# Performance work log

Hardware: AMD Instinct MI355X
Metric: run time of the kernel (lower is better)

## Reference

```python
import jax, jax.numpy as jnp
import numpy as np

N = 64          # Hilbert space dim
B = 4096        # batch of density matrices
K = 2           # number of jump operators
DT = 0.01       # time step
C = (0.0, 0.5, 1.0)
A = ((0.0, 0.0, 0.0), (0.5, 0.0, 0.0), (0.0, 1.0, 0.0))
BW = (1.0 / 6.0, 2.0 / 3.0, 1.0 / 6.0)
NEUMANN_ORDER = 2


def _dag(M):
    # real-valued reference: dagger == transpose on last two axes
    return jnp.swapaxes(M, -1, -2)


def _sandwich(M, rho):
    # M rho M^dag ; M:[N,N], rho:[B,N,N]
    return M @ rho @ _dag(M)


def _dissipator(L, rho):
    # sum_k L_k rho L_k^dag ; L:[K,N,N], rho:[B,N,N]
    return jnp.einsum('kij,bjl,kml->bim', L, rho, L)


def _neumann_ratio(Ui, Uj, I):
    # U(ci) U(cj)^{-1} with U(cj)^{-1} ~ sum_{p<=order} (I - U(cj))^p
    W = I - Uj
    inv = I
    Wp = I
    for _ in range(NEUMANN_ORDER):
        Wp = Wp @ W
        inv = inv + Wp
    return Ui @ inv


def _forward(rho0, U_half, U_one, L0, Lh, L1):
    I = jnp.eye(N, dtype=rho0.dtype)
    Umap = {0.0: I, 0.5: U_half, 1.0: U_one}
    Lmap = {0.0: L0, 0.5: Lh, 1.0: L1}

    def ratio(ci, cj):
        if ci == cj:
            return I
        if cj == 0.0:
            return Umap[ci]
        return _neumann_ratio(Umap[ci], Umap[cj], I)

    # intermediate stages rho^(i)
    stages = []
    for i, ci in enumerate(C):
        rho_i = rho0 if ci == 0.0 else _sandwich(Umap[ci], rho0)
        for j in range(i):
            a_ij = A[i][j]
            if a_ij == 0.0:
                continue
            cj = C[j]
            P_ij = ratio(ci, cj)
            rho_i = rho_i + DT * a_ij * _sandwich(P_ij, _dissipator(Lmap[cj], stages[j]))
        stages.append(rho_i)

    # output combination
    rho_new = _sandwich(Umap[1.0], rho0)
    for i, bi in enumerate(BW):
        if bi == 0.0:
            continue
        ci = C[i]
        Q_i = ratio(1.0, ci)
        rho_new = rho_new + DT * bi * _sandwich(Q_i, _dissipator(Lmap[ci], stages[i]))
    return rho_new


def setup_inputs() -> dict:
    key = jax.random.key(0)
    k1, k2, k3, k4, k5, k6 = jax.random.split(key, 6)
    I = jnp.eye(N, dtype=jnp.float32)
    rho0 = jax.random.normal(k1, (B, N, N), dtype=jnp.float32)
    rho0 = 0.5 * (rho0 + jnp.swapaxes(rho0, -1, -2))  # hermitian-like
    # no-jump propagators: near-identity so the Neumann series is sane
    U_half = I + 0.02 * jax.random.normal(k2, (N, N), dtype=jnp.float32)
    U_one = I + 0.04 * jax.random.normal(k3, (N, N), dtype=jnp.float32)
    L0 = 0.1 * jax.random.normal(k4, (K, N, N), dtype=jnp.float32)
    Lh = 0.1 * jax.random.normal(k5, (K, N, N), dtype=jnp.float32)
    L1 = 0.1 * jax.random.normal(k6, (K, N, N), dtype=jnp.float32)
    return {"rho0": rho0, "U_half": U_half, "U_one": U_one,
            "L0": L0, "Lh": Lh, "L1": L1}


def reference(rho0, U_half, U_one, L0, Lh, L1):
    return _forward(rho0, U_half, U_one, L0, Lh, L1)
```

## Files before the change

### kernel.cpp

```cpp
#include <hip/hip_runtime.h>
#include <hip/hip_bf16.h>

#define NDIM 64
#define BP   72
#define DT_  0.01f
#define NTERM 7

typedef __attribute__((ext_vector_type(8)))  short bf16x8;
typedef __attribute__((ext_vector_type(16))) float f32x16;

struct Frag { bf16x8 f[4]; };


__device__ __forceinline__ unsigned short f2b(float x) {
    __hip_bfloat16 h = __float2bfloat16(x);
    return __builtin_bit_cast(unsigned short, h);
}
__device__ __forceinline__ float b2f(unsigned short u) {
    unsigned int v = (unsigned int)u << 16;
    return __builtin_bit_cast(float, v);
}
__device__ __forceinline__ unsigned int f2b2(float lo, float hi) {
    return (unsigned int)f2b(lo) | ((unsigned int)f2b(hi) << 16);
}

__device__ __forceinline__ void plswap(unsigned int& a, unsigned int& b) {
    asm("v_permlane32_swap_b32 %0, %1" : "+v"(a), "+v"(b));
}


__device__ __forceinline__ bf16x8 ldfrag(const unsigned short* M, int rb, int j, int ln, int hq) {
    return *(const bf16x8*)&M[(rb + ln) * BP + j * 16 + hq * 8];
}

__device__ __forceinline__ void ldg_op(Frag& F, const unsigned short* __restrict__ p,
                                       int ln, int hq, int cw) {
#pragma unroll
    for (int j = 0; j < 4; ++j)
        F.f[j] = *(const bf16x8*)&p[(cw + ln) * 64 + j * 16 + hq * 8];
}

__device__ __forceinline__ void ldsF(Frag& F, const unsigned short* p, int ln, int hq, int cw) {
#pragma unroll
    for (int j = 0; j < 4; ++j)
        F.f[j] = *(const bf16x8*)&p[(cw + ln) * BP + j * 16 + hq * 8];
}

__device__ __forceinline__ void ldg_opF32(Frag& F, const float* __restrict__ P,
                                          int ln, int hq, int cw) {
    const int n = cw + ln;
#pragma unroll
    for (int j = 0; j < 4; ++j) {
        const float* q = &P[n * 64 + j * 16 + hq * 8];
        float4 u = *(const float4*)q;
        float4 v = *(const float4*)(q + 4);
        uint4 o;
        o.x = f2b2(u.x, u.y); o.y = f2b2(u.z, u.w);
        o.z = f2b2(v.x, v.y); o.w = f2b2(v.z, v.w);
        F.f[j] = __builtin_bit_cast(bf16x8, o);
    }
}

__device__ __forceinline__ void ldWfrag(Frag& F, const float* __restrict__ Uh,
                                        int ln, int hq, int cw) {
    const int n = cw + ln;
#pragma unroll
    for (int j = 0; j < 4; ++j) {
        const int k0 = j * 16 + hq * 8;
        const float* q = &Uh[n * 64 + k0];
        float4 u = *(const float4*)q;
        float4 v = *(const float4*)(q + 4);
        float wv[8] = {-u.x, -u.y, -u.z, -u.w, -v.x, -v.y, -v.z, -v.w};
#pragma unroll
        for (int e = 0; e < 8; ++e)
            if (n == k0 + e) wv[e] += 1.f;
        uint4 o;
        o.x = f2b2(wv[0], wv[1]); o.y = f2b2(wv[2], wv[3]);
        o.z = f2b2(wv[4], wv[5]); o.w = f2b2(wv[6], wv[7]);
        F.f[j] = __builtin_bit_cast(bf16x8, o);
    }
}

template <bool ACC>
__device__ __forceinline__ void ntg(const unsigned short* A, const Frag& F, f32x16& acc,
                                    int ln, int hq, int rb) {
    if (!ACC) {
#pragma unroll
        for (int r = 0; r < 16; ++r) acc[r] = 0.f;
    }
#pragma unroll
    for (int j = 0; j < 4; ++j)
        acc = __builtin_amdgcn_mfma_f32_32x32x16_bf16(ldfrag(A, rb, j, ln, hq), F.f[j], acc, 0, 0, 0);
}

__device__ __forceinline__ f32x16 ntg_reg(const Frag& A, const Frag& F, const f32x16& Z) {
    f32x16 a = __builtin_amdgcn_mfma_f32_32x32x16_bf16(A.f[0], F.f[0], Z, 0, 0, 0);
#pragma unroll
    for (int j = 1; j < 4; ++j)
        a = __builtin_amdgcn_mfma_f32_32x32x16_bf16(A.f[j], F.f[j], a, 0, 0, 0);
    return a;
}

__device__ __forceinline__ void stN(unsigned short* D, const f32x16& v,
                                    int ln, int hq, int rw, int cw) {
#pragma unroll
    for (int r = 0; r < 16; ++r) {
        int row = rw + (r & 3) + 8 * (r >> 2) + 4 * hq;
        D[row * BP + (cw + ln)] = f2b(v[r]);
    }
}

__device__ __forceinline__ void ldT(float* r, const unsigned short* S,
                                    int ln, int hq, int rw, int cw) {
#pragma unroll
    for (int g = 0; g < 4; ++g) {
        uint2 u = *(const uint2*)&S[(cw + ln) * BP + rw + 8 * g + 4 * hq];
        unsigned short o[4];
        *(uint2*)o = u;
#pragma unroll
        for (int j = 0; j < 4; ++j) r[4 * g + j] = b2f(o[j]);
    }
}

__device__ __forceinline__ void emit(unsigned short* __restrict__ g, const f32x16& v, float s,
                                     int ln, int hq, int rw, int cw) {
#pragma unroll
    for (int gq = 0; gq < 4; ++gq) {
        uint2 o;
        o.x = f2b2(s * v[4 * gq + 0], s * v[4 * gq + 1]);
        o.y = f2b2(s * v[4 * gq + 2], s * v[4 * gq + 3]);
        *(uint2*)&g[(cw + ln) * 64 + rw + 8 * gq + 4 * hq] = o;
    }
}


__global__ void __launch_bounds__(256) krk_setup(const float* __restrict__ Uh,
                                                 const float* __restrict__ U1,
                                                 const float* __restrict__ L0,
                                                 const float* __restrict__ Lh,
                                                 const float* __restrict__ L1,
                                                 unsigned short* __restrict__ ws) {
    __shared__ unsigned short B[7][NDIM * BP];

    const int tid = threadIdx.x;
    const int lane = tid & 63, w = tid >> 6, ln = lane & 31, hq = lane >> 5;
    const int rw = 32 * (w >> 1), cw = 32 * (w & 1);

    const float c16 = DT_ / 6.f, c23 = 2.f * DT_ / 3.f;
    const float sA = sqrtf(c16);
    const float sB = sqrtf(c23);

#pragma unroll
    for (int i = 0; i < 4; ++i) {
        int flat = (tid + i * 256) * 4;
        int r = flat >> 6, c = flat & 63;
        float4 u = *(const float4*)&Uh[flat];
        const float* uf = (const float*)&u;
        float wv[4];
#pragma unroll
        for (int j = 0; j < 4; ++j) wv[j] = ((r == c + j) ? 1.f : 0.f) - uf[j];
#pragma unroll
        for (int j = 0; j < 4; ++j) B[0][(c + j) * BP + r] = f2b(uf[j]);
        uint2 ow; ow.x = f2b2(wv[0], wv[1]); ow.y = f2b2(wv[2], wv[3]);
        *(uint2*)&B[4][r * BP + c] = ow;
#pragma unroll
        for (int j = 0; j < 4; ++j) B[5][(c + j) * BP + r] = f2b(wv[j]);

        float4 p = *(const float4*)&U1[flat];
        const float* pf = (const float*)&p;
#pragma unroll
        for (int j = 0; j < 4; ++j) B[1][(c + j) * BP + r] = f2b(pf[j]);
        uint2 oq; oq.x = f2b2(p.x, p.y); oq.y = f2b2(p.z, p.w);
        *(uint2*)&ws[flat] = oq;

        float4 a = *(const float4*)&L0[flat];
        const float* af = (const float*)&a;
#pragma unroll
        for (int j = 0; j < 4; ++j) B[2][(c + j) * BP + r] = f2b(af[j]);
        float4 b = *(const float4*)&L0[4096 + flat];
        const float* bf = (const float*)&b;
#pragma unroll
        for (int j = 0; j < 4; ++j) B[3][(c + j) * BP + r] = f2b(bf[j]);
    }

    Frag FUh, FU1, FLh0, FLh1, F10, F11, Fw;
    ldg_opF32(FUh,  Uh,        ln, hq, cw);
    ldg_opF32(FU1,  U1,        ln, hq, cw);
    ldg_opF32(FLh0, Lh,        ln, hq, cw);
    ldg_opF32(FLh1, Lh + 4096, ln, hq, cw);
    ldg_opF32(F10,  L1,        ln, hq, cw);
    ldg_opF32(F11,  L1 + 4096, ln, hq, cw);
    ldWfrag(Fw, Uh, ln, hq, cw);
    __syncthreads();

    f32x16 e;

    {
        f32x16 t0;
        ntg<false>(B[5], Fw, t0, ln, hq, rw);
        float wts[16];
        ldT(wts, B[4], ln, hq, rw, cw);
#pragma unroll
        for (int g = 0; g < 4; ++g) {
            float vv[4];
#pragma unroll
            for (int i = 0; i < 4; ++i) {
                int r = 4 * g + i;
                int row = rw + i + 8 * g + 4 * hq;
                vv[i] = ((row == cw + ln) ? 1.f : 0.f) + wts[r] + t0[r];
            }
            uint2 o; o.x = f2b2(vv[0], vv[1]); o.y = f2b2(vv[2], vv[3]);
            *(uint2*)&B[6][(cw + ln) * BP + rw + 8 * g + 4 * hq] = o;
        }
    }
    ntg<false>(B[2], FU1, e, ln, hq, rw); emit(ws + 1 * 4096, e, sA, ln, hq, rw, cw);
    ntg<false>(B[3], FU1, e, ln, hq, rw); emit(ws + 2 * 4096, e, sA, ln, hq, rw, cw);
    ntg<false>(B[1], F10, e, ln, hq, rw); emit(ws + 5 * 4096, e, sA, ln, hq, rw, cw);
    ntg<false>(B[1], F11, e, ln, hq, rw); emit(ws + 6 * 4096, e, sA, ln, hq, rw, cw);
    __syncthreads();

    Frag FV; ldsF(FV, B[6], ln, hq, cw);

    ntg<false>(B[0], FLh0, e, ln, hq, rw); stN(B[2], e, ln, hq, rw, cw);
    ntg<false>(B[0], FLh1, e, ln, hq, rw); stN(B[3], e, ln, hq, rw, cw);
    __syncthreads();

    ntg<false>(B[2], FV, e, ln, hq, rw); stN(B[4], e, ln, hq, rw, cw);
    ntg<false>(B[3], FV, e, ln, hq, rw); stN(B[5], e, ln, hq, rw, cw);
    __syncthreads();

    ntg<false>(B[4], FU1, e, ln, hq, rw); emit(ws + 3 * 4096, e, sB, ln, hq, rw, cw);
    ntg<false>(B[5], FU1, e, ln, hq, rw); emit(ws + 4 * 4096, e, sB, ln, hq, rw, cw);
}


__global__ void __launch_bounds__(256, 2) krk_main(const float* __restrict__ rho0,
                                                   const unsigned short* __restrict__ ws,
                                                   float* __restrict__ out) {
    const int tid = threadIdx.x;
    const int w = tid >> 6, lane = tid & 63, ln = lane & 31, hq = lane >> 5;

    const int mat = 4 * blockIdx.x + w;
    const float* rho = rho0 + (size_t)mat * 4096;

    Frag Ar[2];
#pragma unroll
    for (int kb = 0; kb < 2; ++kb)
#pragma unroll
        for (int j = 0; j < 4; ++j) {
            const float* q = &rho[(kb * 32 + ln) * 64 + j * 16 + hq * 8];
            float4 u = *(const float4*)q;
            float4 v = *(const float4*)(q + 4);
            uint4 o;
            o.x = f2b2(u.x, u.y); o.y = f2b2(u.z, u.w);
            o.z = f2b2(v.x, v.y); o.w = f2b2(v.z, v.w);
            Ar[kb].f[j] = __builtin_bit_cast(bf16x8, o);
        }

    f32x16 Z;
#pragma unroll
    for (int r = 0; r < 16; ++r) Z[r] = 0.f;
    f32x16 acc00 = Z, acc01 = Z, acc10 = Z, acc11 = Z;

    Frag F[2][2];
    ldg_op(F[0][0], ws, ln, hq, 0);
    ldg_op(F[0][1], ws, ln, hq, 32);

#pragma unroll
    for (int t = 0; t < NTERM; ++t) {
        const int cur = t & 1, nxt = cur ^ 1;
        if (t + 1 < NTERM) {
            ldg_op(F[nxt][0], ws + (size_t)(t + 1) * 4096, ln, hq, 0);
            ldg_op(F[nxt][1], ws + (size_t)(t + 1) * 4096, ln, hq, 32);
        }
#pragma unroll
        for (int c = 0; c < 2; ++c) {
            Frag afr;
#pragma unroll
            for (int kb = 0; kb < 2; ++kb) {
                f32x16 T = ntg_reg(Ar[kb], F[cur][c], Z);
                unsigned int P[8];
#pragma unroll
                for (int p = 0; p < 8; ++p) P[p] = f2b2(T[2 * p], T[2 * p + 1]);
                plswap(P[0], P[2]); plswap(P[1], P[3]);
                plswap(P[4], P[6]); plswap(P[5], P[7]);
                uint4 lo; lo.x = P[0]; lo.y = P[1]; lo.z = P[2]; lo.w = P[3];
                uint4 hi; hi.x = P[4]; hi.y = P[5]; hi.z = P[6]; hi.w = P[7];
                afr.f[2 * kb]     = __builtin_bit_cast(bf16x8, lo);
                afr.f[2 * kb + 1] = __builtin_bit_cast(bf16x8, hi);
            }
#pragma unroll
            for (int j = 0; j < 4; ++j) {
                f32x16& a0 = c ? acc10 : acc00;
                f32x16& a1 = c ? acc11 : acc01;
                a0 = __builtin_amdgcn_mfma_f32_32x32x16_bf16(afr.f[j], F[cur][0].f[j], a0, 0, 0, 0);
                a1 = __builtin_amdgcn_mfma_f32_32x32x16_bf16(afr.f[j], F[cur][1].f[j], a1, 0, 0, 0);
            }
        }
    }

    float* o = out + (size_t)mat * 4096;
#pragma unroll
    for (int I = 0; I < 2; ++I)
#pragma unroll
        for (int J = 0; J < 2; ++J) {
            const f32x16& a = I ? (J ? acc11 : acc10) : (J ? acc01 : acc00);
#pragma unroll
            for (int g = 0; g < 4; ++g) {
                float4 v;
                v.x = a[4 * g + 0]; v.y = a[4 * g + 1];
                v.z = a[4 * g + 2]; v.w = a[4 * g + 3];
                *(float4*)&o[(J * 32 + ln) * 64 + I * 32 + 8 * g + 4 * hq] = v;
            }
        }
}


extern "C" void kernel_launch(void* const* d_in, const int* in_sizes, int n_in,
                              void* d_out, int out_size, void* d_ws, size_t ws_size,
                              hipStream_t stream) {
    const float* rho0 = (const float*)d_in[0];
    const float* Uh   = (const float*)d_in[1];
    const float* U1   = (const float*)d_in[2];
    const float* L0   = (const float*)d_in[3];
    const float* Lh   = (const float*)d_in[4];
    const float* L1   = (const float*)d_in[5];
    float* out = (float*)d_out;
    unsigned short* ws = (unsigned short*)d_ws;

    int Bn = in_sizes[0] / (NDIM * NDIM);

    krk_setup<<<1, 256, 0, stream>>>(Uh, U1, L0, Lh, L1, ws);
    krk_main<<<Bn / 4, 256, 0, stream>>>(rho0, ws, out);
}
```

Before: 161.6 us.

## Split setup across three blocks and split terms across two waves per matrix

The setup kernel is spread over three blocks: one emits the L0 and L1 based factors, the other two each compute one Lh based factor. The main kernel now uses one block of two waves per density matrix. Each wave handles a subset of the seven rank-one terms (4 and 3), and the partial accumulators are reduced through shared memory. This adds parallelism to the serial setup and gives more waves per matrix, at the cost of an LDS reduction and barriers, and with the term work split unevenly between the two waves.

```diff
diff --git a/kernel.cpp b/kernel.cpp
--- a/kernel.cpp
+++ b/kernel.cpp
@@ -142,7 +142,7 @@
                                                  unsigned short* __restrict__ ws) {
     __shared__ unsigned short B[7][NDIM * BP];
 
-    const int tid = threadIdx.x;
+    const int blk = blockIdx.x, tid = threadIdx.x;
     const int lane = tid & 63, w = tid >> 6, ln = lane & 31, hq = lane >> 5;
     const int rw = 32 * (w >> 1), cw = 32 * (w & 1);
 
@@ -171,7 +171,7 @@
 #pragma unroll
         for (int j = 0; j < 4; ++j) B[1][(c + j) * BP + r] = f2b(pf[j]);
         uint2 oq; oq.x = f2b2(p.x, p.y); oq.y = f2b2(p.z, p.w);
-        *(uint2*)&ws[flat] = oq;
+        if (blk == 0) *(uint2*)&ws[flat] = oq;
 
         float4 a = *(const float4*)&L0[flat];
         const float* af = (const float*)&a;
@@ -183,21 +183,30 @@
         for (int j = 0; j < 4; ++j) B[3][(c + j) * BP + r] = f2b(bf[j]);
     }
 
-    Frag FUh, FU1, FLh0, FLh1, F10, F11, Fw;
-    ldg_opF32(FUh,  Uh,        ln, hq, cw);
-    ldg_opF32(FU1,  U1,        ln, hq, cw);
-    ldg_opF32(FLh0, Lh,        ln, hq, cw);
-    ldg_opF32(FLh1, Lh + 4096, ln, hq, cw);
-    ldg_opF32(F10,  L1,        ln, hq, cw);
-    ldg_opF32(F11,  L1 + 4096, ln, hq, cw);
-    ldWfrag(Fw, Uh, ln, hq, cw);
+    Frag FU1, Fa, Fb;
+    ldg_opF32(FU1, U1, ln, hq, cw);
+    if (blk == 0) {
+        ldg_opF32(Fa, L1,        ln, hq, cw);
+        ldg_opF32(Fb, L1 + 4096, ln, hq, cw);
+    } else {
+        ldWfrag(Fa, Uh, ln, hq, cw);
+        ldg_opF32(Fb, (blk == 1) ? Lh : Lh + 4096, ln, hq, cw);
+    }
     __syncthreads();
 
     f32x16 e;
+
+    if (blk == 0) {
+        ntg<false>(B[2], FU1, e, ln, hq, rw); emit(ws + 1 * 4096, e, sA, ln, hq, rw, cw);
+        ntg<false>(B[3], FU1, e, ln, hq, rw); emit(ws + 2 * 4096, e, sA, ln, hq, rw, cw);
+        ntg<false>(B[1], Fa,  e, ln, hq, rw); emit(ws + 5 * 4096, e, sA, ln, hq, rw, cw);
+        ntg<false>(B[1], Fb,  e, ln, hq, rw); emit(ws + 6 * 4096, e, sA, ln, hq, rw, cw);
+        return;
+    }
 
     {
         f32x16 t0;
-        ntg<false>(B[5], Fw, t0, ln, hq, rw);
+        ntg<false>(B[5], Fa, t0, ln, hq, rw);
         float wts[16];
         ldT(wts, B[4], ln, hq, rw, cw);
 #pragma unroll
@@ -213,35 +222,29 @@
             *(uint2*)&B[6][(cw + ln) * BP + rw + 8 * g + 4 * hq] = o;
         }
     }
-    ntg<false>(B[2], FU1, e, ln, hq, rw); emit(ws + 1 * 4096, e, sA, ln, hq, rw, cw);
-    ntg<false>(B[3], FU1, e, ln, hq, rw); emit(ws + 2 * 4096, e, sA, ln, hq, rw, cw);
-    ntg<false>(B[1], F10, e, ln, hq, rw); emit(ws + 5 * 4096, e, sA, ln, hq, rw, cw);
-    ntg<false>(B[1], F11, e, ln, hq, rw); emit(ws + 6 * 4096, e, sA, ln, hq, rw, cw);
+    __syncthreads();
+
+    ntg<false>(B[0], Fb, e, ln, hq, rw); stN(B[2], e, ln, hq, rw, cw);
     __syncthreads();
 
     Frag FV; ldsF(FV, B[6], ln, hq, cw);
-
-    ntg<false>(B[0], FLh0, e, ln, hq, rw); stN(B[2], e, ln, hq, rw, cw);
-    ntg<false>(B[0], FLh1, e, ln, hq, rw); stN(B[3], e, ln, hq, rw, cw);
-    __syncthreads();
-
     ntg<false>(B[2], FV, e, ln, hq, rw); stN(B[4], e, ln, hq, rw, cw);
-    ntg<false>(B[3], FV, e, ln, hq, rw); stN(B[5], e, ln, hq, rw, cw);
-    __syncthreads();
-
-    ntg<false>(B[4], FU1, e, ln, hq, rw); emit(ws + 3 * 4096, e, sB, ln, hq, rw, cw);
-    ntg<false>(B[5], FU1, e, ln, hq, rw); emit(ws + 4 * 4096, e, sB, ln, hq, rw, cw);
-}
-
-
-__global__ void __launch_bounds__(256, 2) krk_main(const float* __restrict__ rho0,
+    __syncthreads();
+
+    ntg<false>(B[4], FU1, e, ln, hq, rw);
+    emit(ws + (size_t)(blk == 1 ? 3 : 4) * 4096, e, sB, ln, hq, rw, cw);
+}
+
+
+__global__ void __launch_bounds__(128, 2) krk_main(const float* __restrict__ rho0,
                                                    const unsigned short* __restrict__ ws,
                                                    float* __restrict__ out) {
+    __shared__ float xch[2][16][64];
+
     const int tid = threadIdx.x;
     const int w = tid >> 6, lane = tid & 63, ln = lane & 31, hq = lane >> 5;
 
-    const int mat = 4 * blockIdx.x + w;
-    const float* rho = rho0 + (size_t)mat * 4096;
+    const float* rho = rho0 + (size_t)blockIdx.x * 4096;
 
     Frag Ar[2];
 #pragma unroll
@@ -262,57 +265,82 @@
     for (int r = 0; r < 16; ++r) Z[r] = 0.f;
     f32x16 acc00 = Z, acc01 = Z, acc10 = Z, acc11 = Z;
 
+    const int tbase = w ? 4 : 0;
+    const int tcnt  = w ? 3 : 4;
+
     Frag F[2][2];
-    ldg_op(F[0][0], ws, ln, hq, 0);
-    ldg_op(F[0][1], ws, ln, hq, 32);
-
-#pragma unroll
-    for (int t = 0; t < NTERM; ++t) {
-        const int cur = t & 1, nxt = cur ^ 1;
-        if (t + 1 < NTERM) {
-            ldg_op(F[nxt][0], ws + (size_t)(t + 1) * 4096, ln, hq, 0);
-            ldg_op(F[nxt][1], ws + (size_t)(t + 1) * 4096, ln, hq, 32);
-        }
-#pragma unroll
-        for (int c = 0; c < 2; ++c) {
-            Frag afr;
-#pragma unroll
-            for (int kb = 0; kb < 2; ++kb) {
-                f32x16 T = ntg_reg(Ar[kb], F[cur][c], Z);
-                unsigned int P[8];
-#pragma unroll
-                for (int p = 0; p < 8; ++p) P[p] = f2b2(T[2 * p], T[2 * p + 1]);
-                plswap(P[0], P[2]); plswap(P[1], P[3]);
-                plswap(P[4], P[6]); plswap(P[5], P[7]);
-                uint4 lo; lo.x = P[0]; lo.y = P[1]; lo.z = P[2]; lo.w = P[3];
-                uint4 hi; hi.x = P[4]; hi.y = P[5]; hi.z = P[6]; hi.w = P[7];
-                afr.f[2 * kb]     = __builtin_bit_cast(bf16x8, lo);
-                afr.f[2 * kb + 1] = __builtin_bit_cast(bf16x8, hi);
+    ldg_op(F[0][0], ws + (size_t)tbase * 4096, ln, hq, 0);
+    ldg_op(F[0][1], ws + (size_t)tbase * 4096, ln, hq, 32);
+
+#pragma unroll
+    for (int i = 0; i < 4; ++i) {
+        if (i < tcnt) {
+            const int cur = i & 1, nxt = cur ^ 1;
+            if (i + 1 < tcnt) {
+                ldg_op(F[nxt][0], ws + (size_t)(tbase + i + 1) * 4096, ln, hq, 0);
+                ldg_op(F[nxt][1], ws + (size_t)(tbase + i + 1) * 4096, ln, hq, 32);
             }
 #pragma unroll
-            for (int j = 0; j < 4; ++j) {
-                f32x16& a0 = c ? acc10 : acc00;
-                f32x16& a1 = c ? acc11 : acc01;
-                a0 = __builtin_amdgcn_mfma_f32_32x32x16_bf16(afr.f[j], F[cur][0].f[j], a0, 0, 0, 0);
-                a1 = __builtin_amdgcn_mfma_f32_32x32x16_bf16(afr.f[j], F[cur][1].f[j], a1, 0, 0, 0);
+            for (int c = 0; c < 2; ++c) {
+                Frag afr;
+#pragma unroll
+                for (int kb = 0; kb < 2; ++kb) {
+                    f32x16 T = ntg_reg(Ar[kb], F[cur][c], Z);
+                    unsigned int P[8];
+#pragma unroll
+                    for (int p = 0; p < 8; ++p) P[p] = f2b2(T[2 * p], T[2 * p + 1]);
+                    plswap(P[0], P[2]); plswap(P[1], P[3]);
+                    plswap(P[4], P[6]); plswap(P[5], P[7]);
+                    uint4 lo; lo.x = P[0]; lo.y = P[1]; lo.z = P[2]; lo.w = P[3];
+                    uint4 hi; hi.x = P[4]; hi.y = P[5]; hi.z = P[6]; hi.w = P[7];
+                    afr.f[2 * kb]     = __builtin_bit_cast(bf16x8, lo);
+                    afr.f[2 * kb + 1] = __builtin_bit_cast(bf16x8, hi);
+                }
+#pragma unroll
+                for (int j = 0; j < 4; ++j) {
+                    f32x16& a0 = c ? acc10 : acc00;
+                    f32x16& a1 = c ? acc11 : acc01;
+                    a0 = __builtin_amdgcn_mfma_f32_32x32x16_bf16(afr.f[j], F[cur][0].f[j], a0, 0, 0, 0);
+                    a1 = __builtin_amdgcn_mfma_f32_32x32x16_bf16(afr.f[j], F[cur][1].f[j], a1, 0, 0, 0);
+                }
             }
         }
     }
 
-    float* o = out + (size_t)mat * 4096;
-#pragma unroll
-    for (int I = 0; I < 2; ++I)
-#pragma unroll
-        for (int J = 0; J < 2; ++J) {
-            const f32x16& a = I ? (J ? acc11 : acc10) : (J ? acc01 : acc00);
-#pragma unroll
-            for (int g = 0; g < 4; ++g) {
-                float4 v;
-                v.x = a[4 * g + 0]; v.y = a[4 * g + 1];
-                v.z = a[4 * g + 2]; v.w = a[4 * g + 3];
-                *(float4*)&o[(J * 32 + ln) * 64 + I * 32 + 8 * g + 4 * hq] = v;
+    if (w == 1) {
+#pragma unroll
+        for (int r = 0; r < 16; ++r) { xch[0][r][lane] = acc00[r]; xch[1][r][lane] = acc01[r]; }
+    }
+    __syncthreads();
+    if (w == 0) {
+#pragma unroll
+        for (int r = 0; r < 16; ++r) { acc00[r] += xch[0][r][lane]; acc01[r] += xch[1][r][lane]; }
+    }
+    __syncthreads();
+    if (w == 1) {
+#pragma unroll
+        for (int r = 0; r < 16; ++r) { xch[0][r][lane] = acc10[r]; xch[1][r][lane] = acc11[r]; }
+    }
+    __syncthreads();
+    if (w == 0) {
+#pragma unroll
+        for (int r = 0; r < 16; ++r) { acc10[r] += xch[0][r][lane]; acc11[r] += xch[1][r][lane]; }
+
+        float* o = out + (size_t)blockIdx.x * 4096;
+#pragma unroll
+        for (int I = 0; I < 2; ++I)
+#pragma unroll
+            for (int J = 0; J < 2; ++J) {
+                const f32x16& a = I ? (J ? acc11 : acc10) : (J ? acc01 : acc00);
+#pragma unroll
+                for (int g = 0; g < 4; ++g) {
+                    float4 v;
+                    v.x = a[4 * g + 0]; v.y = a[4 * g + 1];
+                    v.z = a[4 * g + 2]; v.w = a[4 * g + 3];
+                    *(float4*)&o[(J * 32 + ln) * 64 + I * 32 + 8 * g + 4 * hq] = v;
+                }
             }
-        }
+    }
 }
 
 
@@ -330,6 +358,6 @@
 
     int Bn = in_sizes[0] / (NDIM * NDIM);
 
-    krk_setup<<<1, 256, 0, stream>>>(Uh, U1, L0, Lh, L1, ws);
-    krk_main<<<Bn / 4, 256, 0, stream>>>(rho0, ws, out);
-}
+    krk_setup<<<3, 256, 0, stream>>>(Uh, U1, L0, Lh, L1, ws);
+    krk_main<<<Bn, 128, 0, stream>>>(rho0, ws, out);
+}
```

Result: no change. 164.0 us (+1.5%).
